# Performance work log

Measured on AMD Instinct MI355X. Metric: run time of the kernel, lower is better.

Reference implementation:

```python
import jax, jax.numpy as jnp
import numpy as np

HIDDEN = 5120
N_HEADS = 16           # 128 total heads / DEVICE_NUM=8
Q_LORA = 1536
KV_LORA = 512
NOPE = 128
ROPE = 64
QK_DIM = NOPE + ROPE   # 192
V_DIM = 128
EPS = 1e-6
ROPE_BASE = 10000.0
SCALE_BY_DEVICE = 1.0 / 8.0
SOFTMAX_SCALE = QK_DIM ** -0.5
B, S = 1, 2048


def rms_norm(x, w, eps=EPS):
    v = jnp.mean(jnp.square(x), axis=-1, keepdims=True)
    return x * jax.lax.rsqrt(v + eps) * w


def rotate_half(x):
    h = x.shape[-1] // 2
    return jnp.concatenate([-x[..., h:], x[..., :h]], axis=-1)


def interleave(x):
    # DeepSeek rope layout: view(b,h,s,d//2,2).transpose(-1,-2).reshape(b,h,s,d)
    b, h, s, d = x.shape
    return jnp.swapaxes(x.reshape(b, h, s, d // 2, 2), -1, -2).reshape(b, h, s, d)


def setup_inputs() -> dict:
    key = jax.random.key(0)
    ks = jax.random.split(key, 8)
    w = 0.02
    hidden_states = jax.random.normal(ks[0], (B, S, HIDDEN), dtype=jnp.float32)
    position_ids = jnp.arange(S, dtype=jnp.int64 if jax.config.jax_enable_x64 else jnp.int32)[None, :]
    causal = jnp.tril(jnp.ones((S, S), dtype=bool))
    attention_mask = jnp.where(causal, 0.0, -1e9).astype(jnp.float32)[None, None]
    return {
        'hidden_states': hidden_states,
        'position_ids': position_ids,
        'attention_mask': attention_mask,
        'ln_w': jnp.ones((HIDDEN,), jnp.float32),
        'wq_a': jax.random.normal(ks[1], (Q_LORA, HIDDEN), jnp.float32) * w,
        'q_a_ln_w': jnp.ones((Q_LORA,), jnp.float32),
        'wq_b': jax.random.normal(ks[2], (N_HEADS * QK_DIM, Q_LORA), jnp.float32) * w,
        'wkv_a': jax.random.normal(ks[3], (KV_LORA + ROPE, HIDDEN), jnp.float32) * w,
        'kv_a_ln_w': jnp.ones((KV_LORA,), jnp.float32),
        'wkv_b': jax.random.normal(ks[4], (N_HEADS * (NOPE + V_DIM), KV_LORA), jnp.float32) * w,
        'wo': jax.random.normal(ks[5], (HIDDEN, N_HEADS * V_DIM), jnp.float32) * w,
    }


def reference(hidden_states, position_ids, attention_mask, ln_w, wq_a, q_a_ln_w,
              wq_b, wkv_a, kv_a_ln_w, wkv_b, wo):
    b, s, _ = hidden_states.shape
    residual = hidden_states * SCALE_BY_DEVICE
    h = rms_norm(hidden_states, ln_w)

    # Q low-rank decompression: q_a_proj -> RMSNorm -> q_b_proj
    q = rms_norm(h @ wq_a.T, q_a_ln_w) @ wq_b.T
    q = q.reshape(b, s, N_HEADS, QK_DIM).transpose(0, 2, 1, 3)  # b,h,s,192
    q_nope, q_pe = q[..., :NOPE], q[..., NOPE:]

    # KV low-rank: kv_a_proj_with_mqa -> split -> RMSNorm -> kv_b_proj
    ckv = h @ wkv_a.T                                           # b,s,512+64
    c_kv, k_pe = ckv[..., :KV_LORA], ckv[..., KV_LORA:]
    k_pe = k_pe[:, None, :, :]                                  # b,1,s,64
    kv = rms_norm(c_kv, kv_a_ln_w) @ wkv_b.T
    kv = kv.reshape(b, s, N_HEADS, NOPE + V_DIM).transpose(0, 2, 1, 3)
    k_nope, v = kv[..., :NOPE], kv[..., NOPE:]

    # RoPE (DeepSeek interleaved layout)
    inv_freq = 1.0 / (ROPE_BASE ** (jnp.arange(0, ROPE, 2, dtype=jnp.float32) / ROPE))
    freqs = position_ids.astype(jnp.float32)[..., None] * inv_freq  # b,s,32
    emb = jnp.concatenate([freqs, freqs], axis=-1)                  # b,s,64
    cos = jnp.cos(emb)[:, None]                                     # b,1,s,64
    sin = jnp.sin(emb)[:, None]
    q_pe = interleave(q_pe)
    k_pe = interleave(k_pe)
    q_pe = q_pe * cos + rotate_half(q_pe) * sin
    k_pe = k_pe * cos + rotate_half(k_pe) * sin

    k = jnp.concatenate([k_nope, jnp.broadcast_to(k_pe, (b, N_HEADS, s, ROPE))], axis=-1)
    qf = jnp.concatenate([q_nope, q_pe], axis=-1)

    scores = jnp.einsum('bhqd,bhkd->bhqk', qf, k) * SOFTMAX_SCALE + attention_mask
    attn = jax.nn.softmax(scores.astype(jnp.float32), axis=-1).astype(qf.dtype)
    out = jnp.einsum('bhqk,bhkd->bhqd', attn, v)                    # b,h,s,128
    out = out.transpose(0, 2, 1, 3).reshape(b, s, N_HEADS * V_DIM) @ wo.T

    hidden_states = residual + out
    return (hidden_states.astype(jnp.float32), k.astype(jnp.float32), v.astype(jnp.float32))
```

## Files before the change

kernel.cpp:

```cpp
#include <hip/hip_runtime.h>
#include <hip/hip_bf16.h>

typedef __hip_bfloat16 bf16;
typedef __attribute__((ext_vector_type(8))) short bf16x8;
typedef __attribute__((ext_vector_type(4))) float f32x4;

#define S_LEN   2048
#define HIDDEN  5120
#define NHEADS  16
#define QLORA   1536
#define KVLORA  512
#define QKD     192
#define VD      128
#define QN      (NHEADS*QKD)
#define KVN     (NHEADS*(128+VD))
#define QCKN    2112
#define SM_SCALE 0.07216878364870322f

__device__ __forceinline__ f32x4 mfma16(bf16x8 a, bf16x8 b, f32x4 c) {
  return __builtin_amdgcn_mfma_f32_16x16x32_bf16(a, b, c, 0, 0, 0);
}
__device__ __forceinline__ void g2l16(const void* g, void* l) {
  __builtin_amdgcn_global_load_lds((const __attribute__((address_space(1))) void*)g,
                                   (__attribute__((address_space(3))) void*)l, 16, 0, 0);
}
__device__ __forceinline__ bf16x8 ld8(const bf16* p) { return *(const bf16x8*)p; }

__global__ void cvt_multi(const float* s0, bf16* d0, int n0,
                          const float* s1, bf16* d1, int n1,
                          const float* s2, bf16* d2, int n2,
                          const float* s3, bf16* d3, int n3,
                          const float* s4, bf16* d4, int n4s)
{
  int i = blockIdx.x * 256 + threadIdx.x;
  const float* s; bf16* d;
  if (i < n0) { s = s0; d = d0; }
  else if ((i -= n0) < n1) { s = s1; d = d1; }
  else if ((i -= n1) < n2) { s = s2; d = d2; }
  else if ((i -= n2) < n3) { s = s3; d = d3; }
  else if ((i -= n3) < n4s) { s = s4; d = d4; }
  else return;
  const float4 v = ((const float4*)s)[i];
  union { bf16 b[4]; unsigned long long u; } pk;
  pk.b[0] = __float2bfloat16(v.x);
  pk.b[1] = __float2bfloat16(v.y);
  pk.b[2] = __float2bfloat16(v.z);
  pk.b[3] = __float2bfloat16(v.w);
  *(unsigned long long*)(d + (size_t)i * 4) = pk.u;
}

__global__ void rmsnorm_k(const float* __restrict__ in, int istride, int C,
                          const float* __restrict__ w,
                          bf16* __restrict__ out, int ostride)
{
  const int row = blockIdx.x;
  const float* x = in + (size_t)row * istride;
  float ss = 0.f;
  for (int c = threadIdx.x; c < C; c += 256) { float v = x[c]; ss += v * v; }
  #pragma unroll
  for (int m = 32; m >= 1; m >>= 1) ss += __shfl_xor(ss, m, 64);
  __shared__ float red[4];
  if ((threadIdx.x & 63) == 0) red[threadIdx.x >> 6] = ss;
  __syncthreads();
  ss = red[0] + red[1] + red[2] + red[3];
  const float sc = rsqrtf(ss / (float)C + 1e-6f);
  bf16* o = out + (size_t)row * ostride;
  for (int c = threadIdx.x; c < C; c += 256)
    o[c] = __float2bfloat16(x[c] * sc * w[c]);
}

__global__ void rmsnorm2_k(const float* __restrict__ parts,
                           const float* __restrict__ wq, const float* __restrict__ wk,
                           bf16* __restrict__ qa_n, bf16* __restrict__ ckv_n,
                           float* __restrict__ kpe_sum)
{
  const int r = blockIdx.x;
  const bool is_q = r < S_LEN;
  const int row = is_q ? r : r - S_LEN;
  const int C = is_q ? QLORA : KVLORA;
  const size_t PS = (size_t)S_LEN * QCKN;
  const float* x0 = parts + (size_t)row * QCKN + (is_q ? 0 : QLORA);
  const float* w = is_q ? wq : wk;
  bf16* o = (is_q ? qa_n + (size_t)row * QLORA : ckv_n + (size_t)row * KVLORA);
  __shared__ float xs[QLORA];
  float ss = 0.f;
  for (int c = threadIdx.x; c < C; c += 256) {
    const float v = x0[c] + x0[PS + c] + x0[2 * PS + c] + x0[3 * PS + c];
    xs[c] = v;
    ss += v * v;
  }
  #pragma unroll
  for (int m = 32; m >= 1; m >>= 1) ss += __shfl_xor(ss, m, 64);
  __shared__ float red[4];
  if ((threadIdx.x & 63) == 0) red[threadIdx.x >> 6] = ss;
  __syncthreads();
  ss = red[0] + red[1] + red[2] + red[3];
  const float sc = rsqrtf(ss / (float)C + 1e-6f);
  for (int c = threadIdx.x; c < C; c += 256)
    o[c] = __float2bfloat16(xs[c] * sc * w[c]);
  if (!is_q) {
    const float* kp = parts + (size_t)row * QCKN + 2048;
    for (int c = threadIdx.x; c < 64; c += 256)
      kpe_sum[row * 64 + c] = kp[c] + kp[PS + c] + kp[2 * PS + c] + kp[3 * PS + c];
  }
}

template<bool RESID, bool CLAMPN, bool SPLIT>
__global__ __launch_bounds__(256, 4)
void gemm_nt(const bf16* __restrict__ A, const bf16* __restrict__ Bt,
             float* __restrict__ C, int M, int N, int lda, int klen,
             const float* __restrict__ resid, float rscale)
{
  __shared__ bf16 As[2 * 128 * 32];
  __shared__ bf16 Bs[2 * 128 * 32];
  const int tid = threadIdx.x;
  const int wave = tid >> 6;
  const int lane = tid & 63;
  const int l15 = lane & 15, quad = lane >> 4;
  const int bm = blockIdx.x * 128, bn = blockIdx.y * 128;
  const int kbase = blockIdx.z * klen;
  const int wm = (wave >> 1) * 64, wn = (wave & 1) * 64;

  const int srow = tid >> 2;
  const int scol = (((tid & 3) ^ ((tid >> 3) & 3)) << 3);
  const bf16* Ag0 = A + (size_t)(bm + srow) * lda + kbase + scol;
  const bf16* Ag1 = A + (size_t)(bm + 64 + srow) * lda + kbase + scol;
  int bn0 = bn + srow, bn1 = bn + 64 + srow;
  if (CLAMPN) { bn0 = min(bn0, N - 1); bn1 = min(bn1, N - 1); }
  const bf16* Bg0 = Bt + (size_t)bn0 * lda + kbase + scol;
  const bf16* Bg1 = Bt + (size_t)bn1 * lda + kbase + scol;

  char* AsW = (char*)As + wave * 1024;
  char* BsW = (char*)Bs + wave * 1024;

  const int qs = ((quad ^ ((l15 >> 1) & 3)) << 3);

  f32x4 acc[4][4];
  #pragma unroll
  for (int i = 0; i < 4; i++)
    #pragma unroll
    for (int j = 0; j < 4; j++) acc[i][j] = (f32x4){0.f, 0.f, 0.f, 0.f};

  const int nk = klen >> 6;
  for (int kt = 0; kt < nk; ++kt) {
    const int k0 = kt << 6;
    #pragma unroll
    for (int c = 0; c < 2; ++c) {
      g2l16(Ag0 + k0 + c * 32, AsW + c * 8192);
      g2l16(Ag1 + k0 + c * 32, AsW + c * 8192 + 4096);
      g2l16(Bg0 + k0 + c * 32, BsW + c * 8192);
      g2l16(Bg1 + k0 + c * 32, BsW + c * 8192 + 4096);
    }
    __syncthreads();
    #pragma unroll
    for (int c = 0; c < 2; ++c) {
      bf16x8 af[4], bfr[4];
      #pragma unroll
      for (int i = 0; i < 4; i++)
        af[i] = ld8(As + c * 4096 + (wm + i * 16 + l15) * 32 + qs);
      #pragma unroll
      for (int j = 0; j < 4; j++)
        bfr[j] = ld8(Bs + c * 4096 + (wn + j * 16 + l15) * 32 + qs);
      #pragma unroll
      for (int i = 0; i < 4; i++)
        #pragma unroll
        for (int j = 0; j < 4; j++)
          acc[i][j] = mfma16(af[i], bfr[j], acc[i][j]);
    }
    __syncthreads();
  }

  float* Cb = C;
  if (SPLIT) Cb += (size_t)blockIdx.z * ((size_t)S_LEN * (size_t)N);
  #pragma unroll
  for (int i = 0; i < 4; i++)
    #pragma unroll
    for (int j = 0; j < 4; j++) {
      const int row = bm + wm + i * 16 + quad * 4;
      const int col = bn + wn + j * 16 + l15;
      if (!CLAMPN || col < N) {
        #pragma unroll
        for (int r = 0; r < 4; r++) {
          float v = acc[i][j][r];
          const size_t idx = (size_t)(row + r) * N + col;
          if (RESID) v += resid[idx] * rscale;
          Cb[idx] = v;
        }
      }
    }
}

__global__ void rope_assemble_k(
    const float* __restrict__ qp,
    const float* __restrict__ kpe_sum,
    const float* __restrict__ kv,
    const int*   __restrict__ pos,
    float* __restrict__ k_out,
    bf16*  __restrict__ q_bf,
    bf16*  __restrict__ k_bf)
{
  const int s = blockIdx.x;
  const int t = threadIdx.x;
  const size_t QPS = (size_t)S_LEN * QN;
  __shared__ float cs[32], sn[32], kpe[64];
  const float p = (float)pos[s];
  if (t < 32) {
    const float inv = powf(10000.0f, -((float)(2 * t)) / 64.0f);
    const float f = p * inv;
    float si, c;
    sincosf(f, &si, &c);
    cs[t] = c; sn[t] = si;
    const float r0v = kpe_sum[(size_t)s * 64 + 2 * t];
    const float r1v = kpe_sum[(size_t)s * 64 + 2 * t + 1];
    kpe[t]      = r0v * c - r1v * si;
    kpe[32 + t] = r1v * c + r0v * si;
  }
  __syncthreads();
  for (int i = t; i < NHEADS * 128; i += 256) {
    const int h = i >> 7, d = i & 127;
    const size_t o = ((size_t)h * S_LEN + s) * QKD + d;
    const float kn = kv[(size_t)s * KVN + h * 256 + d];
    k_out[o] = kn;
    k_bf[o] = __float2bfloat16(kn);
    const size_t qi = (size_t)s * QN + h * QKD + d;
    q_bf[o] = __float2bfloat16(qp[qi] + qp[QPS + qi]);
  }
  for (int i = t; i < NHEADS * 32; i += 256) {
    const int h = i >> 5, jj = i & 31;
    const size_t qi = (size_t)s * QN + h * QKD + 128 + 2 * jj;
    const float r0v = qp[qi] + qp[QPS + qi];
    const float r1v = qp[qi + 1] + qp[QPS + qi + 1];
    const float c = cs[jj], si = sn[jj];
    const size_t o = ((size_t)h * S_LEN + s) * QKD + 128;
    q_bf[o + jj]      = __float2bfloat16(r0v * c - r1v * si);
    q_bf[o + 32 + jj] = __float2bfloat16(r1v * c + r0v * si);
  }
  for (int i = t; i < NHEADS * 64; i += 256) {
    const int h = i >> 6, jj = i & 63;
    const float v = kpe[jj];
    const size_t o = ((size_t)h * S_LEN + s) * QKD + 128 + jj;
    k_out[o] = v;
    k_bf[o] = __float2bfloat16(v);
  }
}

__global__ void v_transpose_k(const float* __restrict__ kv,
                              float* __restrict__ v_out,
                              bf16* __restrict__ vt_bf)
{
  const int h = blockIdx.x, st = blockIdx.y, dt = blockIdx.z;
  __shared__ float tile[32][33];
  const int tx = threadIdx.x & 31;
  const int ty = (threadIdx.x >> 5) * 4;
  const int s0 = st * 32, d0 = dt * 32;
  #pragma unroll
  for (int r = 0; r < 4; r++) {
    const int sl = ty + r;
    const float v = kv[(size_t)(s0 + sl) * KVN + h * 256 + 128 + d0 + tx];
    v_out[((size_t)h * S_LEN + s0 + sl) * VD + d0 + tx] = v;
    tile[sl][tx] = v;
  }
  __syncthreads();
  #pragma unroll
  for (int r = 0; r < 4; r++) {
    const int dl = ty + r;
    vt_bf[((size_t)h * VD + d0 + dl) * S_LEN + s0 + tx] = __float2bfloat16(tile[tx][dl]);
  }
}

__global__ __launch_bounds__(256, 3)
void attn_k(const bf16* __restrict__ qb, const bf16* __restrict__ kb,
            const bf16* __restrict__ vt, bf16* __restrict__ aout)
{
  const int lin = blockIdx.x + blockIdx.y * 32;
  const int xcd = lin & 7;
  const int idx = lin >> 3;
  const int head = xcd * 2 + (idx >> 5);
  const int qt = (idx >> 5) ? (31 - (idx & 31)) : (idx & 31);
  const int wave = threadIdx.x >> 6, lane = threadIdx.x & 63;
  const int l15 = lane & 15, quad = lane >> 4;
  const int r0 = qt * 64 + wave * 16;

  const bf16* qh = qb + (size_t)head * S_LEN * QKD;
  const bf16* kh = kb + (size_t)head * S_LEN * QKD;
  const bf16* vh = vt + (size_t)head * VD * S_LEN;

  __shared__ bf16 Ks[6 * 64 * 32];
  __shared__ bf16 Vs[128 * 72];
  __shared__ bf16 Plds[4][16][72];

  const int tid = threadIdx.x;
  const int srow = wave * 16 + (lane >> 2);
  const int scol = (lane & 3) * 8;
  const bf16* ksrc = kh + (size_t)srow * QKD + scol;
  bf16* kdst = Ks + srow * 32 + (((lane & 3) ^ ((lane >> 3) & 3)) << 3);
  const int vrow = tid >> 1;
  const int vcol = (tid & 1) * 32;
  const bf16* vsrc = vh + (size_t)vrow * S_LEN + vcol;
  bf16* vdst = Vs + vrow * 72 + vcol;

  const int qs = ((quad ^ ((l15 >> 1) & 3)) << 3);

  bf16x8 qf[6];
  #pragma unroll
  for (int c = 0; c < 6; ++c)
    qf[c] = ld8(qh + (size_t)(r0 + l15) * QKD + c * 32 + quad * 8);

  f32x4 O[8];
  #pragma unroll
  for (int d = 0; d < 8; ++d) O[d] = (f32x4){0.f, 0.f, 0.f, 0.f};
  float mrow[4] = {-1e30f, -1e30f, -1e30f, -1e30f};
  float lrow[4] = {0.f, 0.f, 0.f, 0.f};

  bf16x8 kreg[6], vreg[4];
  #pragma unroll
  for (int c = 0; c < 6; ++c) kreg[c] = ld8(ksrc + c * 32);
  #pragma unroll
  for (int c = 0; c < 4; ++c) vreg[c] = ld8(vsrc + c * 8);

  for (int j = 0; j <= qt; ++j) {
    __syncthreads();
    #pragma unroll
    for (int c = 0; c < 6; ++c) *(bf16x8*)(kdst + c * 2048) = kreg[c];
    #pragma unroll
    for (int c = 0; c < 4; ++c) *(bf16x8*)(vdst + c * 8) = vreg[c];
    __syncthreads();
    if (j < qt) {
      const bf16* src = ksrc + (size_t)(j + 1) * 64 * QKD;
      #pragma unroll
      for (int c = 0; c < 6; ++c) kreg[c] = ld8(src + c * 32);
      const bf16* vs2 = vsrc + (size_t)(j + 1) * 64;
      #pragma unroll
      for (int c = 0; c < 4; ++c) vreg[c] = ld8(vs2 + c * 8);
    }
    const int kc = j * 64;

    f32x4 S[4];
    #pragma unroll
    for (int nt = 0; nt < 4; ++nt) S[nt] = (f32x4){0.f, 0.f, 0.f, 0.f};
    #pragma unroll
    for (int c = 0; c < 6; ++c) {
      #pragma unroll
      for (int nt = 0; nt < 4; ++nt) {
        const bf16x8 kf = ld8(Ks + c * 2048 + (nt * 16 + l15) * 32 + qs);
        S[nt] = mfma16(qf[c], kf, S[nt]);
      }
    }

    float mnew[4] = {-1e30f, -1e30f, -1e30f, -1e30f};
    if (j == qt) {
      #pragma unroll
      for (int nt = 0; nt < 4; ++nt) {
        const int col = kc + nt * 16 + l15;
        #pragma unroll
        for (int r = 0; r < 4; r++) {
          const int row = r0 + quad * 4 + r;
          const float v = (col <= row) ? S[nt][r] * SM_SCALE : -1e30f;
          S[nt][r] = v;
          mnew[r] = fmaxf(mnew[r], v);
        }
      }
    } else {
      #pragma unroll
      for (int nt = 0; nt < 4; ++nt)
        #pragma unroll
        for (int r = 0; r < 4; r++) {
          const float v = S[nt][r] * SM_SCALE;
          S[nt][r] = v;
          mnew[r] = fmaxf(mnew[r], v);
        }
    }
    #pragma unroll
    for (int m = 8; m >= 1; m >>= 1)
      #pragma unroll
      for (int r = 0; r < 4; r++)
        mnew[r] = fmaxf(mnew[r], __shfl_xor(mnew[r], m, 64));
    float alpha[4], ladd[4] = {0.f, 0.f, 0.f, 0.f};
    #pragma unroll
    for (int r = 0; r < 4; r++) {
      const float mi = fmaxf(mrow[r], mnew[r]);
      alpha[r] = __expf(mrow[r] - mi);
      mrow[r] = mi;
    }
    #pragma unroll
    for (int nt = 0; nt < 4; ++nt)
      #pragma unroll
      for (int r = 0; r < 4; r++) {
        const float pv = __expf(S[nt][r] - mrow[r]);
        S[nt][r] = pv;
        ladd[r] += pv;
      }
    #pragma unroll
    for (int m = 8; m >= 1; m >>= 1)
      #pragma unroll
      for (int r = 0; r < 4; r++) ladd[r] += __shfl_xor(ladd[r], m, 64);
    #pragma unroll
    for (int r = 0; r < 4; r++) lrow[r] = lrow[r] * alpha[r] + ladd[r];
    #pragma unroll
    for (int d = 0; d < 8; ++d)
      #pragma unroll
      for (int r = 0; r < 4; r++) O[d][r] *= alpha[r];

    #pragma unroll
    for (int nt = 0; nt < 4; ++nt)
      #pragma unroll
      for (int r = 0; r < 4; r++)
        Plds[wave][quad * 4 + r][nt * 16 + l15] = __float2bfloat16(S[nt][r]);

    #pragma unroll
    for (int kt = 0; kt < 2; ++kt) {
      const bf16x8 pf = ld8(&Plds[wave][l15][kt * 32 + quad * 8]);
      #pragma unroll
      for (int dt = 0; dt < 8; ++dt) {
        const bf16x8 vf = ld8(Vs + (dt * 16 + l15) * 72 + kt * 32 + quad * 8);
        O[dt] = mfma16(pf, vf, O[dt]);
      }
    }
  }

  #pragma unroll
  for (int dt = 0; dt < 8; ++dt) {
    const int col = head * VD + dt * 16 + l15;
    #pragma unroll
    for (int r = 0; r < 4; r++) {
      const int row = r0 + quad * 4 + r;
      aout[(size_t)row * (NHEADS * VD) + col] = __float2bfloat16(O[dt][r] / lrow[r]);
    }
  }
}

extern "C" void kernel_launch(void* const* d_in, const int* in_sizes, int n_in,
                              void* d_out, int out_size, void* d_ws, size_t ws_size,
                              hipStream_t stream)
{
  const float* hs      = (const float*)d_in[0];
  const int*   pos     = (const int*)  d_in[1];
  const float* ln_w    = (const float*)d_in[3];
  const float* wq_a    = (const float*)d_in[4];
  const float* q_a_ln  = (const float*)d_in[5];
  const float* wq_b    = (const float*)d_in[6];
  const float* wkv_a   = (const float*)d_in[7];
  const float* kv_a_ln = (const float*)d_in[8];
  const float* wkv_b   = (const float*)d_in[9];
  const float* wo      = (const float*)d_in[10];

  float* out_hidden = (float*)d_out;
  float* out_k = out_hidden + (size_t)S_LEN * HIDDEN;
  float* out_v = out_k + (size_t)NHEADS * S_LEN * QKD;

  char* ws = (char*)d_ws;
  size_t off = 0;
  auto alloc = [&](size_t bytes) { char* p = ws + off; off += (bytes + 255) & ~255ULL; return p; };

  bf16* h_b     = (bf16*)alloc((size_t)S_LEN * HIDDEN * 2);
  bf16* w1_b    = (bf16*)alloc((size_t)QCKN * HIDDEN * 2);
  bf16* wqb_b   = (bf16*)alloc((size_t)QN * QLORA * 2);
  bf16* wkvb_b  = (bf16*)alloc((size_t)KVN * KVLORA * 2);
  bf16* wo_b    = (bf16*)alloc((size_t)HIDDEN * (NHEADS * VD) * 2);
  char* region  = alloc((size_t)2 * S_LEN * QN * 4 + (size_t)S_LEN * KVN * 4);
  float* qa_parts = (float*)region;
  float* q_f      = (float*)region;
  float* kv_f     = (float*)(region + (size_t)2 * S_LEN * QN * 4);
  float* kpe_sum = (float*)alloc((size_t)S_LEN * 64 * 4);
  bf16* qa_n    = (bf16*)alloc((size_t)S_LEN * QLORA * 2);
  bf16* ckv_n   = (bf16*)alloc((size_t)S_LEN * KVLORA * 2);
  bf16* q_bf    = (bf16*)alloc((size_t)NHEADS * S_LEN * QKD * 2);
  bf16* k_bf    = (bf16*)alloc((size_t)NHEADS * S_LEN * QKD * 2);
  bf16* vt_bf   = (bf16*)alloc((size_t)NHEADS * VD * S_LEN * 2);
  bf16* attn_b  = (bf16*)alloc((size_t)S_LEN * (NHEADS * VD) * 2);

  {
    const int n0 = (QLORA * HIDDEN) / 4;
    const int n1 = ((QCKN - QLORA) * HIDDEN) / 4;
    const int n2 = (QN * QLORA) / 4;
    const int n3 = (KVN * KVLORA) / 4;
    const int n4s = (HIDDEN * NHEADS * VD) / 4;
    const int tot = n0 + n1 + n2 + n3 + n4s;
    cvt_multi<<<(tot + 255) / 256, 256, 0, stream>>>(
        wq_a, w1_b, n0,
        wkv_a, w1_b + (size_t)QLORA * HIDDEN, n1,
        wq_b, wqb_b, n2,
        wkv_b, wkvb_b, n3,
        wo, wo_b, n4s);
  }

  rmsnorm_k<<<S_LEN, 256, 0, stream>>>(hs, HIDDEN, HIDDEN, ln_w, h_b, HIDDEN);

  gemm_nt<false, true, true><<<dim3(16, 17, 4), 256, 0, stream>>>(
      h_b, w1_b, qa_parts, S_LEN, QCKN, HIDDEN, HIDDEN / 4, nullptr, 0.f);

  rmsnorm2_k<<<2 * S_LEN, 256, 0, stream>>>(qa_parts, q_a_ln, kv_a_ln,
                                            qa_n, ckv_n, kpe_sum);

  gemm_nt<false, false, true><<<dim3(16, QN / 128, 2), 256, 0, stream>>>(
      qa_n, wqb_b, q_f, S_LEN, QN, QLORA, QLORA / 2, nullptr, 0.f);
  gemm_nt<false, false, false><<<dim3(16, KVN / 128, 1), 256, 0, stream>>>(
      ckv_n, wkvb_b, kv_f, S_LEN, KVN, KVLORA, KVLORA, nullptr, 0.f);

  rope_assemble_k<<<S_LEN, 256, 0, stream>>>(q_f, kpe_sum, kv_f, pos,
                                             out_k, q_bf, k_bf);
  v_transpose_k<<<dim3(NHEADS, S_LEN / 32, VD / 32), 256, 0, stream>>>(kv_f, out_v, vt_bf);

  attn_k<<<dim3(S_LEN / 64, NHEADS), 256, 0, stream>>>(q_bf, k_bf, vt_bf, attn_b);

  gemm_nt<true, false, false><<<dim3(16, HIDDEN / 128, 1), 256, 0, stream>>>(
      attn_b, wo_b, out_hidden, S_LEN, HIDDEN, NHEADS * VD, NHEADS * VD, hs, 0.125f);

  (void)in_sizes; (void)n_in; (void)out_size; (void)ws_size;
}
```

Measured before the change: 539.1 us.

## Pair low and high causal query tiles per block to share K/V loads

Each attention block now processes two query tiles, qt=b and 31-b, of the same head. K/V tiles are loaded into shared memory once and reused by both tiles while the low tile is still active. This balances causal work across blocks and halves the number of blocks to 256, one per CU. Register pressure roughly doubles (two sets of Q fragments and O accumulators), so launch bounds drop to 1 block per CU, which lowers occupancy.

```diff
diff --git a/kernel.cpp b/kernel.cpp
--- a/kernel.cpp
+++ b/kernel.cpp
@@ -268,18 +268,65 @@
   }
 }
 
-__global__ __launch_bounds__(256, 3)
+#define SMAX(Sx, mr, lr, Ox, r0x, slot, isdiag)                               \
+  do {                                                                        \
+    float mnew[4] = {-1e30f, -1e30f, -1e30f, -1e30f};                         \
+    if (isdiag) {                                                             \
+      _Pragma("unroll") for (int nt = 0; nt < 4; ++nt) {                      \
+        const int col = kc + nt * 16 + l15;                                   \
+        _Pragma("unroll") for (int r = 0; r < 4; r++) {                       \
+          const int row = (r0x) + quad * 4 + r;                               \
+          const float v = (col <= row) ? Sx[nt][r] * SM_SCALE : -1e30f;       \
+          Sx[nt][r] = v; mnew[r] = fmaxf(mnew[r], v);                         \
+        }                                                                     \
+      }                                                                       \
+    } else {                                                                  \
+      _Pragma("unroll") for (int nt = 0; nt < 4; ++nt)                        \
+        _Pragma("unroll") for (int r = 0; r < 4; r++) {                       \
+          const float v = Sx[nt][r] * SM_SCALE;                               \
+          Sx[nt][r] = v; mnew[r] = fmaxf(mnew[r], v);                         \
+        }                                                                     \
+    }                                                                         \
+    _Pragma("unroll") for (int mm = 8; mm >= 1; mm >>= 1)                     \
+      _Pragma("unroll") for (int r = 0; r < 4; r++)                           \
+        mnew[r] = fmaxf(mnew[r], __shfl_xor(mnew[r], mm, 64));                \
+    float alpha[4], ladd[4] = {0.f, 0.f, 0.f, 0.f};                           \
+    _Pragma("unroll") for (int r = 0; r < 4; r++) {                           \
+      const float mi = fmaxf(mr[r], mnew[r]);                                 \
+      alpha[r] = __expf(mr[r] - mi); mr[r] = mi;                              \
+    }                                                                         \
+    _Pragma("unroll") for (int nt = 0; nt < 4; ++nt)                          \
+      _Pragma("unroll") for (int r = 0; r < 4; r++) {                         \
+        const float pv = __expf(Sx[nt][r] - mr[r]);                           \
+        Sx[nt][r] = pv; ladd[r] += pv;                                        \
+      }                                                                       \
+    _Pragma("unroll") for (int mm = 8; mm >= 1; mm >>= 1)                     \
+      _Pragma("unroll") for (int r = 0; r < 4; r++)                           \
+        ladd[r] += __shfl_xor(ladd[r], mm, 64);                               \
+    _Pragma("unroll") for (int r = 0; r < 4; r++)                             \
+      lr[r] = lr[r] * alpha[r] + ladd[r];                                     \
+    _Pragma("unroll") for (int d = 0; d < 8; ++d)                             \
+      _Pragma("unroll") for (int r = 0; r < 4; r++) Ox[d][r] *= alpha[r];     \
+    _Pragma("unroll") for (int nt = 0; nt < 4; ++nt)                          \
+      _Pragma("unroll") for (int r = 0; r < 4; r++)                           \
+        Plds[slot][wave][quad * 4 + r][nt * 16 + l15] =                       \
+            __float2bfloat16(Sx[nt][r]);                                      \
+  } while (0)
+
+__global__ __launch_bounds__(256, 1)
 void attn_k(const bf16* __restrict__ qb, const bf16* __restrict__ kb,
             const bf16* __restrict__ vt, bf16* __restrict__ aout)
 {
-  const int lin = blockIdx.x + blockIdx.y * 32;
+  const int lin = blockIdx.x;
   const int xcd = lin & 7;
   const int idx = lin >> 3;
-  const int head = xcd * 2 + (idx >> 5);
-  const int qt = (idx >> 5) ? (31 - (idx & 31)) : (idx & 31);
+  const int head = xcd * 2 + (idx >> 4);
+  const int b = idx & 15;
+  const int qtl = b, qth = 31 - b;
   const int wave = threadIdx.x >> 6, lane = threadIdx.x & 63;
   const int l15 = lane & 15, quad = lane >> 4;
-  const int r0 = qt * 64 + wave * 16;
+  const int r0l = qtl * 64 + wave * 16;
+  const int r0h = qth * 64 + wave * 16;
 
   const bf16* qh = qb + (size_t)head * S_LEN * QKD;
   const bf16* kh = kb + (size_t)head * S_LEN * QKD;
@@ -287,7 +334,7 @@
 
   __shared__ bf16 Ks[6 * 64 * 32];
   __shared__ bf16 Vs[128 * 72];
-  __shared__ bf16 Plds[4][16][72];
+  __shared__ bf16 Plds[2][4][16][72];
 
   const int tid = threadIdx.x;
   const int srow = wave * 16 + (lane >> 2);
@@ -301,16 +348,23 @@
 
   const int qs = ((quad ^ ((l15 >> 1) & 3)) << 3);
 
-  bf16x8 qf[6];
-  #pragma unroll
-  for (int c = 0; c < 6; ++c)
-    qf[c] = ld8(qh + (size_t)(r0 + l15) * QKD + c * 32 + quad * 8);
-
-  f32x4 O[8];
-  #pragma unroll
-  for (int d = 0; d < 8; ++d) O[d] = (f32x4){0.f, 0.f, 0.f, 0.f};
-  float mrow[4] = {-1e30f, -1e30f, -1e30f, -1e30f};
-  float lrow[4] = {0.f, 0.f, 0.f, 0.f};
+  bf16x8 qfh[6], qfl[6];
+  #pragma unroll
+  for (int c = 0; c < 6; ++c) {
+    qfh[c] = ld8(qh + (size_t)(r0h + l15) * QKD + c * 32 + quad * 8);
+    qfl[c] = ld8(qh + (size_t)(r0l + l15) * QKD + c * 32 + quad * 8);
+  }
+
+  f32x4 Oh[8], Ol[8];
+  #pragma unroll
+  for (int d = 0; d < 8; ++d) {
+    Oh[d] = (f32x4){0.f, 0.f, 0.f, 0.f};
+    Ol[d] = (f32x4){0.f, 0.f, 0.f, 0.f};
+  }
+  float mh[4] = {-1e30f, -1e30f, -1e30f, -1e30f};
+  float ml[4] = {-1e30f, -1e30f, -1e30f, -1e30f};
+  float lh[4] = {0.f, 0.f, 0.f, 0.f};
+  float ll[4] = {0.f, 0.f, 0.f, 0.f};
 
   bf16x8 kreg[6], vreg[4];
   #pragma unroll
@@ -318,14 +372,14 @@
   #pragma unroll
   for (int c = 0; c < 4; ++c) vreg[c] = ld8(vsrc + c * 8);
 
-  for (int j = 0; j <= qt; ++j) {
+  for (int j = 0; j <= qth; ++j) {
     __syncthreads();
     #pragma unroll
     for (int c = 0; c < 6; ++c) *(bf16x8*)(kdst + c * 2048) = kreg[c];
     #pragma unroll
     for (int c = 0; c < 4; ++c) *(bf16x8*)(vdst + c * 8) = vreg[c];
     __syncthreads();
-    if (j < qt) {
+    if (j < qth) {
       const bf16* src = ksrc + (size_t)(j + 1) * 64 * QKD;
       #pragma unroll
       for (int c = 0; c < 6; ++c) kreg[c] = ld8(src + c * 32);
@@ -335,85 +389,54 @@
     }
     const int kc = j * 64;
 
-    f32x4 S[4];
-    #pragma unroll
-    for (int nt = 0; nt < 4; ++nt) S[nt] = (f32x4){0.f, 0.f, 0.f, 0.f};
-    #pragma unroll
-    for (int c = 0; c < 6; ++c) {
+    if (j <= qtl) {
+      f32x4 Sh[4], Sl[4];
       #pragma unroll
       for (int nt = 0; nt < 4; ++nt) {
-        const bf16x8 kf = ld8(Ks + c * 2048 + (nt * 16 + l15) * 32 + qs);
-        S[nt] = mfma16(qf[c], kf, S[nt]);
+        Sh[nt] = (f32x4){0.f, 0.f, 0.f, 0.f};
+        Sl[nt] = (f32x4){0.f, 0.f, 0.f, 0.f};
       }
-    }
-
-    float mnew[4] = {-1e30f, -1e30f, -1e30f, -1e30f};
-    if (j == qt) {
-      #pragma unroll
-      for (int nt = 0; nt < 4; ++nt) {
-        const int col = kc + nt * 16 + l15;
+      #pragma unroll
+      for (int c = 0; c < 6; ++c)
         #pragma unroll
-        for (int r = 0; r < 4; r++) {
-          const int row = r0 + quad * 4 + r;
-          const float v = (col <= row) ? S[nt][r] * SM_SCALE : -1e30f;
-          S[nt][r] = v;
-          mnew[r] = fmaxf(mnew[r], v);
+        for (int nt = 0; nt < 4; ++nt) {
+          const bf16x8 kf = ld8(Ks + c * 2048 + (nt * 16 + l15) * 32 + qs);
+          Sh[nt] = mfma16(qfh[c], kf, Sh[nt]);
+          Sl[nt] = mfma16(qfl[c], kf, Sl[nt]);
+        }
+      SMAX(Sh, mh, lh, Oh, r0h, 0, false);
+      SMAX(Sl, ml, ll, Ol, r0l, 1, j == qtl);
+      #pragma unroll
+      for (int kt = 0; kt < 2; ++kt) {
+        const bf16x8 pfh = ld8(&Plds[0][wave][l15][kt * 32 + quad * 8]);
+        const bf16x8 pfl = ld8(&Plds[1][wave][l15][kt * 32 + quad * 8]);
+        #pragma unroll
+        for (int dt = 0; dt < 8; ++dt) {
+          const bf16x8 vf = ld8(Vs + (dt * 16 + l15) * 72 + kt * 32 + quad * 8);
+          Oh[dt] = mfma16(pfh, vf, Oh[dt]);
+          Ol[dt] = mfma16(pfl, vf, Ol[dt]);
         }
       }
     } else {
-      #pragma unroll
-      for (int nt = 0; nt < 4; ++nt)
+      f32x4 Sh[4];
+      #pragma unroll
+      for (int nt = 0; nt < 4; ++nt) Sh[nt] = (f32x4){0.f, 0.f, 0.f, 0.f};
+      #pragma unroll
+      for (int c = 0; c < 6; ++c)
         #pragma unroll
-        for (int r = 0; r < 4; r++) {
-          const float v = S[nt][r] * SM_SCALE;
-          S[nt][r] = v;
-          mnew[r] = fmaxf(mnew[r], v);
+        for (int nt = 0; nt < 4; ++nt) {
+          const bf16x8 kf = ld8(Ks + c * 2048 + (nt * 16 + l15) * 32 + qs);
+          Sh[nt] = mfma16(qfh[c], kf, Sh[nt]);
         }
-    }
-    #pragma unroll
-    for (int m = 8; m >= 1; m >>= 1)
-      #pragma unroll
-      for (int r = 0; r < 4; r++)
-        mnew[r] = fmaxf(mnew[r], __shfl_xor(mnew[r], m, 64));
-    float alpha[4], ladd[4] = {0.f, 0.f, 0.f, 0.f};
-    #pragma unroll
-    for (int r = 0; r < 4; r++) {
-      const float mi = fmaxf(mrow[r], mnew[r]);
-      alpha[r] = __expf(mrow[r] - mi);
-      mrow[r] = mi;
-    }
-    #pragma unroll
-    for (int nt = 0; nt < 4; ++nt)
-      #pragma unroll
-      for (int r = 0; r < 4; r++) {
-        const float pv = __expf(S[nt][r] - mrow[r]);
-        S[nt][r] = pv;
-        ladd[r] += pv;
-      }
-    #pragma unroll
-    for (int m = 8; m >= 1; m >>= 1)
-      #pragma unroll
-      for (int r = 0; r < 4; r++) ladd[r] += __shfl_xor(ladd[r], m, 64);
-    #pragma unroll
-    for (int r = 0; r < 4; r++) lrow[r] = lrow[r] * alpha[r] + ladd[r];
-    #pragma unroll
-    for (int d = 0; d < 8; ++d)
-      #pragma unroll
-      for (int r = 0; r < 4; r++) O[d][r] *= alpha[r];
-
-    #pragma unroll
-    for (int nt = 0; nt < 4; ++nt)
-      #pragma unroll
-      for (int r = 0; r < 4; r++)
-        Plds[wave][quad * 4 + r][nt * 16 + l15] = __float2bfloat16(S[nt][r]);
-
-    #pragma unroll
-    for (int kt = 0; kt < 2; ++kt) {
-      const bf16x8 pf = ld8(&Plds[wave][l15][kt * 32 + quad * 8]);
-      #pragma unroll
-      for (int dt = 0; dt < 8; ++dt) {
-        const bf16x8 vf = ld8(Vs + (dt * 16 + l15) * 72 + kt * 32 + quad * 8);
-        O[dt] = mfma16(pf, vf, O[dt]);
+      SMAX(Sh, mh, lh, Oh, r0h, 0, j == qth);
+      #pragma unroll
+      for (int kt = 0; kt < 2; ++kt) {
+        const bf16x8 pfh = ld8(&Plds[0][wave][l15][kt * 32 + quad * 8]);
+        #pragma unroll
+        for (int dt = 0; dt < 8; ++dt) {
+          const bf16x8 vf = ld8(Vs + (dt * 16 + l15) * 72 + kt * 32 + quad * 8);
+          Oh[dt] = mfma16(pfh, vf, Oh[dt]);
+        }
       }
     }
   }
@@ -423,8 +446,10 @@
     const int col = head * VD + dt * 16 + l15;
     #pragma unroll
     for (int r = 0; r < 4; r++) {
-      const int row = r0 + quad * 4 + r;
-      aout[(size_t)row * (NHEADS * VD) + col] = __float2bfloat16(O[dt][r] / lrow[r]);
+      const int rowh = r0h + quad * 4 + r;
+      const int rowl = r0l + quad * 4 + r;
+      aout[(size_t)rowh * (NHEADS * VD) + col] = __float2bfloat16(Oh[dt][r] / lh[r]);
+      aout[(size_t)rowl * (NHEADS * VD) + col] = __float2bfloat16(Ol[dt][r] / ll[r]);
     }
   }
 }
@@ -501,7 +526,7 @@
                                              out_k, q_bf, k_bf);
   v_transpose_k<<<dim3(NHEADS, S_LEN / 32, VD / 32), 256, 0, stream>>>(kv_f, out_v, vt_bf);
 
-  attn_k<<<dim3(S_LEN / 64, NHEADS), 256, 0, stream>>>(q_bf, k_bf, vt_bf, attn_b);
+  attn_k<<<dim3(256), 256, 0, stream>>>(q_bf, k_bf, vt_bf, attn_b);
 
   gemm_nt<true, false, false><<<dim3(16, HIDDEN / 128, 1), 256, 0, stream>>>(
       attn_b, wo_b, out_hidden, S_LEN, HIDDEN, NHEADS * VD, NHEADS * VD, hs, 0.125f);
```

Result: no change. 539.7 us (+0.1%).

## Split long causal attention tiles across two blocks and merge partials

Applied to the files above, without the earlier changes.

The attention kernel now gives each block an equal share of causal work. The upper-half query tiles are split at KV tile 16: one block does KV tiles 0-15, and a second block does a short low query tile plus the rest of the high tile. Partial O, max and sum values go to fp32 scratch, and a new merge kernel combines them with log-sum-exp rescaling. The aim is to remove the long-tail imbalance of causal attention, at the cost of an extra launch, partial-result traffic and a lower occupancy hint (2 instead of 3).

```diff
diff --git a/kernel.cpp b/kernel.cpp
--- a/kernel.cpp
+++ b/kernel.cpp
@@ -268,28 +268,19 @@
   }
 }
 
-__global__ __launch_bounds__(256, 3)
-void attn_k(const bf16* __restrict__ qb, const bf16* __restrict__ kb,
-            const bf16* __restrict__ vt, bf16* __restrict__ aout)
-{
-  const int lin = blockIdx.x + blockIdx.y * 32;
-  const int xcd = lin & 7;
-  const int idx = lin >> 3;
-  const int head = xcd * 2 + (idx >> 5);
-  const int qt = (idx >> 5) ? (31 - (idx & 31)) : (idx & 31);
-  const int wave = threadIdx.x >> 6, lane = threadIdx.x & 63;
+template<bool PARTIAL>
+__device__ __forceinline__ void attn_tile(
+    const bf16* __restrict__ qh, const bf16* __restrict__ kh,
+    const bf16* __restrict__ vh,
+    bf16* Ks, bf16* Vs, bf16* Plds,
+    int qt, int j0, int j1, int head,
+    bf16* __restrict__ aout, float* __restrict__ Op, float* __restrict__ Ml)
+{
+  const int tid = threadIdx.x;
+  const int wave = tid >> 6, lane = tid & 63;
   const int l15 = lane & 15, quad = lane >> 4;
   const int r0 = qt * 64 + wave * 16;
 
-  const bf16* qh = qb + (size_t)head * S_LEN * QKD;
-  const bf16* kh = kb + (size_t)head * S_LEN * QKD;
-  const bf16* vh = vt + (size_t)head * VD * S_LEN;
-
-  __shared__ bf16 Ks[6 * 64 * 32];
-  __shared__ bf16 Vs[128 * 72];
-  __shared__ bf16 Plds[4][16][72];
-
-  const int tid = threadIdx.x;
   const int srow = wave * 16 + (lane >> 2);
   const int scol = (lane & 3) * 8;
   const bf16* ksrc = kh + (size_t)srow * QKD + scol;
@@ -298,7 +289,6 @@
   const int vcol = (tid & 1) * 32;
   const bf16* vsrc = vh + (size_t)vrow * S_LEN + vcol;
   bf16* vdst = Vs + vrow * 72 + vcol;
-
   const int qs = ((quad ^ ((l15 >> 1) & 3)) << 3);
 
   bf16x8 qf[6];
@@ -314,18 +304,18 @@
 
   bf16x8 kreg[6], vreg[4];
   #pragma unroll
-  for (int c = 0; c < 6; ++c) kreg[c] = ld8(ksrc + c * 32);
-  #pragma unroll
-  for (int c = 0; c < 4; ++c) vreg[c] = ld8(vsrc + c * 8);
-
-  for (int j = 0; j <= qt; ++j) {
+  for (int c = 0; c < 6; ++c) kreg[c] = ld8(ksrc + (size_t)j0 * 64 * QKD + c * 32);
+  #pragma unroll
+  for (int c = 0; c < 4; ++c) vreg[c] = ld8(vsrc + (size_t)j0 * 64 + c * 8);
+
+  for (int j = j0; j < j1; ++j) {
     __syncthreads();
     #pragma unroll
     for (int c = 0; c < 6; ++c) *(bf16x8*)(kdst + c * 2048) = kreg[c];
     #pragma unroll
     for (int c = 0; c < 4; ++c) *(bf16x8*)(vdst + c * 8) = vreg[c];
     __syncthreads();
-    if (j < qt) {
+    if (j + 1 < j1) {
       const bf16* src = ksrc + (size_t)(j + 1) * 64 * QKD;
       #pragma unroll
       for (int c = 0; c < 6; ++c) kreg[c] = ld8(src + c * 32);
@@ -339,13 +329,12 @@
     #pragma unroll
     for (int nt = 0; nt < 4; ++nt) S[nt] = (f32x4){0.f, 0.f, 0.f, 0.f};
     #pragma unroll
-    for (int c = 0; c < 6; ++c) {
+    for (int c = 0; c < 6; ++c)
       #pragma unroll
       for (int nt = 0; nt < 4; ++nt) {
         const bf16x8 kf = ld8(Ks + c * 2048 + (nt * 16 + l15) * 32 + qs);
         S[nt] = mfma16(qf[c], kf, S[nt]);
       }
-    }
 
     float mnew[4] = {-1e30f, -1e30f, -1e30f, -1e30f};
     if (j == qt) {
@@ -405,11 +394,12 @@
     for (int nt = 0; nt < 4; ++nt)
       #pragma unroll
       for (int r = 0; r < 4; r++)
-        Plds[wave][quad * 4 + r][nt * 16 + l15] = __float2bfloat16(S[nt][r]);
+        Plds[(wave * 16 + quad * 4 + r) * 72 + nt * 16 + l15] =
+            __float2bfloat16(S[nt][r]);
 
     #pragma unroll
     for (int kt = 0; kt < 2; ++kt) {
-      const bf16x8 pf = ld8(&Plds[wave][l15][kt * 32 + quad * 8]);
+      const bf16x8 pf = ld8(Plds + (wave * 16 + l15) * 72 + kt * 32 + quad * 8);
       #pragma unroll
       for (int dt = 0; dt < 8; ++dt) {
         const bf16x8 vf = ld8(Vs + (dt * 16 + l15) * 72 + kt * 32 + quad * 8);
@@ -418,14 +408,96 @@
     }
   }
 
-  #pragma unroll
-  for (int dt = 0; dt < 8; ++dt) {
-    const int col = head * VD + dt * 16 + l15;
-    #pragma unroll
-    for (int r = 0; r < 4; r++) {
-      const int row = r0 + quad * 4 + r;
-      aout[(size_t)row * (NHEADS * VD) + col] = __float2bfloat16(O[dt][r] / lrow[r]);
-    }
+  if (PARTIAL) {
+    #pragma unroll
+    for (int dt = 0; dt < 8; ++dt)
+      #pragma unroll
+      for (int r = 0; r < 4; r++)
+        Op[(wave * 16 + quad * 4 + r) * 128 + dt * 16 + l15] = O[dt][r];
+    if (l15 == 0) {
+      #pragma unroll
+      for (int r = 0; r < 4; r++) {
+        Ml[wave * 16 + quad * 4 + r] = mrow[r];
+        Ml[64 + wave * 16 + quad * 4 + r] = lrow[r];
+      }
+    }
+  } else {
+    #pragma unroll
+    for (int dt = 0; dt < 8; ++dt) {
+      const int col = head * VD + dt * 16 + l15;
+      #pragma unroll
+      for (int r = 0; r < 4; r++) {
+        const int row = r0 + quad * 4 + r;
+        aout[(size_t)row * (NHEADS * VD) + col] = __float2bfloat16(O[dt][r] / lrow[r]);
+      }
+    }
+  }
+}
+
+__global__ __launch_bounds__(256, 2)
+void attn_k(const bf16* __restrict__ qb, const bf16* __restrict__ kb,
+            const bf16* __restrict__ vt, bf16* __restrict__ aout,
+            float* __restrict__ Opart, float* __restrict__ Mlpart)
+{
+  __shared__ bf16 Ks[6 * 64 * 32];
+  __shared__ bf16 Vs[128 * 72];
+  __shared__ bf16 Plds[4 * 16 * 72];
+
+  const int lin = blockIdx.x;
+  const int xcd = lin & 7;
+  const int t = lin >> 3;
+  const int head = xcd * 2 + (t >> 5);
+  const int rem = t & 31;
+  const int b = rem >> 1;
+  const int role = rem & 1;
+  const int qtl = b, qth = 31 - b;
+  const int pi = head * 16 + (15 - b);
+
+  const bf16* qh = qb + (size_t)head * S_LEN * QKD;
+  const bf16* kh = kb + (size_t)head * S_LEN * QKD;
+  const bf16* vh = vt + (size_t)head * VD * S_LEN;
+
+  if (role == 0) {
+    attn_tile<true>(qh, kh, vh, Ks, Vs, Plds, qth, 0, 16, head, aout,
+                    Opart + (size_t)pi * 8192, Mlpart + (size_t)pi * 128);
+  } else {
+    attn_tile<false>(qh, kh, vh, Ks, Vs, Plds, qtl, 0, qtl + 1, head, aout,
+                     nullptr, nullptr);
+    attn_tile<true>(qh, kh, vh, Ks, Vs, Plds, qth, 16, qth + 1, head, aout,
+                    Opart + (size_t)(256 + pi) * 8192,
+                    Mlpart + (size_t)(256 + pi) * 128);
+  }
+}
+
+__global__ void merge_k(const float* __restrict__ Opart,
+                        const float* __restrict__ Mlpart,
+                        bf16* __restrict__ aout)
+{
+  const int pi = blockIdx.x;
+  const int head = pi >> 4;
+  const int qth = (pi & 15) + 16;
+  const int tid = threadIdx.x;
+  const int r = tid >> 2;
+  const int d0 = (tid & 3) * 32;
+  const float mA = Mlpart[(size_t)pi * 128 + r];
+  const float lA = Mlpart[(size_t)pi * 128 + 64 + r];
+  const float mB = Mlpart[(size_t)(256 + pi) * 128 + r];
+  const float lB = Mlpart[(size_t)(256 + pi) * 128 + 64 + r];
+  const float m = fmaxf(mA, mB);
+  const float fa = __expf(mA - m), fb = __expf(mB - m);
+  const float inv = 1.f / (lA * fa + lB * fb);
+  const float4* OA = (const float4*)(Opart + (size_t)pi * 8192 + r * 128 + d0);
+  const float4* OB = (const float4*)(Opart + (size_t)(256 + pi) * 8192 + r * 128 + d0);
+  bf16* out = aout + (size_t)(qth * 64 + r) * (NHEADS * VD) + head * VD + d0;
+  #pragma unroll
+  for (int i = 0; i < 8; ++i) {
+    const float4 va = OA[i], vb = OB[i];
+    union { bf16 h[4]; unsigned long long u; } pk;
+    pk.h[0] = __float2bfloat16((va.x * fa + vb.x * fb) * inv);
+    pk.h[1] = __float2bfloat16((va.y * fa + vb.y * fb) * inv);
+    pk.h[2] = __float2bfloat16((va.z * fa + vb.z * fb) * inv);
+    pk.h[3] = __float2bfloat16((va.w * fa + vb.w * fb) * inv);
+    *(unsigned long long*)(out + i * 4) = pk.u;
   }
 }
 
@@ -461,6 +533,8 @@
   float* qa_parts = (float*)region;
   float* q_f      = (float*)region;
   float* kv_f     = (float*)(region + (size_t)2 * S_LEN * QN * 4);
+  float* Opart    = (float*)region;
+  float* Mlpart   = (float*)(region + (size_t)512 * 8192 * 4);
   float* kpe_sum = (float*)alloc((size_t)S_LEN * 64 * 4);
   bf16* qa_n    = (bf16*)alloc((size_t)S_LEN * QLORA * 2);
   bf16* ckv_n   = (bf16*)alloc((size_t)S_LEN * KVLORA * 2);
@@ -501,7 +575,8 @@
                                              out_k, q_bf, k_bf);
   v_transpose_k<<<dim3(NHEADS, S_LEN / 32, VD / 32), 256, 0, stream>>>(kv_f, out_v, vt_bf);
 
-  attn_k<<<dim3(S_LEN / 64, NHEADS), 256, 0, stream>>>(q_bf, k_bf, vt_bf, attn_b);
+  attn_k<<<dim3(512), 256, 0, stream>>>(q_bf, k_bf, vt_bf, attn_b, Opart, Mlpart);
+  merge_k<<<dim3(256), 256, 0, stream>>>(Opart, Mlpart, attn_b);
 
   gemm_nt<true, false, false><<<dim3(16, HIDDEN / 128, 1), 256, 0, stream>>>(
       attn_b, wo_b, out_hidden, S_LEN, HIDDEN, NHEADS * VD, NHEADS * VD, hs, 0.125f);
```

Result: faster. 519.3 us (-3.7%).
